# Kernel tuning notes

Hardware: AMD Instinct MI355X
Metric: run time of the kernel (lower is better)

The kernel has to match this reference:

```python
import jax, jax.numpy as jnp
import numpy as np

N_NODES = 50000
N_EDGES = 800000
NODE_FEAT = 3
EDGE_FEAT = 2
EMBED = 64
HIDDEN = 128
LAYERS = 4
POLY = 8


def setup_inputs() -> dict:
    key = jax.random.key(0)
    ks = jax.random.split(key, 24)
    s = 0.05
    inp = {
        "node_features": jax.random.normal(ks[0], (N_NODES, NODE_FEAT), jnp.float32),
        "edge_index": jax.random.randint(ks[1], (2, N_EDGES), 0, N_NODES, jnp.int32),
        "edge_features": jax.random.normal(ks[2], (N_EDGES, EDGE_FEAT), jnp.float32),
        "n": N_NODES,
        # node encoder MLP
        "enc_w1": jax.random.normal(ks[3], (NODE_FEAT, HIDDEN), jnp.float32) * s,
        "enc_b1": jnp.zeros((HIDDEN,), jnp.float32),
        "enc_w2": jax.random.normal(ks[4], (HIDDEN, EMBED), jnp.float32) * s,
        "enc_b2": jnp.zeros((EMBED,), jnp.float32),
        # per-layer conv message MLP (stacked over layers)
        "conv_w1": jax.random.normal(ks[5], (LAYERS, 2 * EMBED + EDGE_FEAT, EMBED), jnp.float32) * s,
        "conv_b1": jnp.zeros((LAYERS, EMBED), jnp.float32),
        "conv_w2": jax.random.normal(ks[6], (LAYERS, EMBED, EMBED), jnp.float32) * s,
        "conv_b2": jnp.zeros((LAYERS, EMBED), jnp.float32),
        # per-layer skip linear and layernorm
        "skip_w": jax.random.normal(ks[7], (LAYERS, EMBED, EMBED), jnp.float32) * s,
        "skip_b": jnp.zeros((LAYERS, EMBED), jnp.float32),
        "ln_g": jnp.ones((LAYERS, EMBED), jnp.float32),
        "ln_b": jnp.zeros((LAYERS, EMBED), jnp.float32),
        # polynomial head
        "head_w1": jax.random.normal(ks[8], (EMBED, EMBED), jnp.float32) * s,
        "head_b1": jnp.zeros((EMBED,), jnp.float32),
        "head_w2": jnp.zeros((EMBED, POLY), jnp.float32),  # zero-init per module
        "head_b2": jnp.ones((POLY,), jnp.float32),         # bias filled with 1.0
    }
    return inp


def _layernorm(x, g, b, eps=1e-5):
    mu = jnp.mean(x, axis=-1, keepdims=True)
    var = jnp.var(x, axis=-1, keepdims=True)
    return (x - mu) * jax.lax.rsqrt(var + eps) * g + b


def reference(node_features, edge_index, edge_features, n,
              enc_w1, enc_b1, enc_w2, enc_b2,
              conv_w1, conv_b1, conv_w2, conv_b2,
              skip_w, skip_b, ln_g, ln_b,
              head_w1, head_b1, head_w2, head_b2):
    rows, cols = edge_index[0], edge_index[1]
    # node encoder
    h = jax.nn.relu(node_features @ enc_w1 + enc_b1) @ enc_w2 + enc_b2  # [n, E]
    L = conv_w1.shape[0]
    for i in range(L):
        # gather + concat: [E_edges, 2*embed + edge_feat]
        msg_in = jnp.concatenate([h[rows], h[cols], edge_features], axis=-1)
        msg = jax.nn.relu(msg_in @ conv_w1[i] + conv_b1[i]) @ conv_w2[i] + conv_b2[i]
        agg = jax.ops.segment_sum(msg, rows, num_segments=n)  # scatter_add over source rows
        h_new = agg + h @ skip_w[i] + skip_b[i]
        h = jax.nn.relu(_layernorm(h_new, ln_g[i], ln_b[i]))
    # polynomial head
    return jax.nn.relu(h @ head_w1 + head_b1) @ head_w2 + head_b2  # [n, poly_degree]
```

## Files before the change

### kernel.cpp

```cpp
#include <hip/hip_runtime.h>

typedef unsigned short u16;
typedef __attribute__((ext_vector_type(8))) short bf16x8;
typedef __attribute__((ext_vector_type(4))) float f32x4;

#define MFMA16(a,b,c) __builtin_amdgcn_mfma_f32_16x16x32_bf16((a),(b),(c),0,0,0)

static __device__ __forceinline__ u16 f2bf(float x){
    unsigned int u = __float_as_uint(x);
    u += 0x7FFFu + ((u >> 16) & 1u);
    return (u16)(u >> 16);
}
static __device__ __forceinline__ float bf2f(short s){
    return __uint_as_float(((unsigned int)(u16)s) << 16);
}

static __device__ __forceinline__ bf16x8 load_bfrag(const float* __restrict__ W, int ldn, int n, int k0){
    bf16x8 r;
    #pragma unroll
    for (int j = 0; j < 8; ++j) r[j] = (short)f2bf(W[(k0 + j) * ldn + n]);
    return r;
}

__global__ __launch_bounds__(256) void enc_kernel(
    const float* __restrict__ X, const float* __restrict__ W1, const float* __restrict__ B1,
    const float* __restrict__ W2, const float* __restrict__ B2,
    const float* __restrict__ cW1, const float* __restrict__ cB1,
    u16* __restrict__ hbf, u16* __restrict__ Ubf, u16* __restrict__ Vbf, int N)
{
    __shared__ u16 sHid[64 * 136];
    __shared__ u16 sH[64 * 72];
    const int tid = threadIdx.x;
    const int w = tid >> 6, l = tid & 63, l15 = l & 15, quad = l >> 4;

    bf16x8 bW[4][4];
    #pragma unroll
    for (int ks = 0; ks < 4; ++ks)
        #pragma unroll
        for (int f = 0; f < 4; ++f)
            bW[ks][f] = load_bfrag(W2, 64, f * 16 + l15, ks * 32 + quad * 8);
    float b2v[4];
    #pragma unroll
    for (int f = 0; f < 4; ++f) b2v[f] = B2[f * 16 + l15];

    const int nbase = blockIdx.x * 64 + w * 16;

    {
        int e = l >> 2;
        int node = nbase + e; if (node > N - 1) node = N - 1;
        float x0 = X[node * 3], x1 = X[node * 3 + 1], x2 = X[node * 3 + 2];
        int k0 = (l & 3) * 32;
        u16* dst = sHid + (w * 16 + e) * 136 + k0;
        #pragma unroll
        for (int j = 0; j < 32; ++j){
            int k = k0 + j;
            float hv = x0 * W1[k] + x1 * W1[128 + k] + x2 * W1[256 + k] + B1[k];
            dst[j] = f2bf(hv > 0.f ? hv : 0.f);
        }
    }

    f32x4 acc[4];
    #pragma unroll
    for (int f = 0; f < 4; ++f){ acc[f][0]=b2v[f]; acc[f][1]=b2v[f]; acc[f][2]=b2v[f]; acc[f][3]=b2v[f]; }
    #pragma unroll
    for (int ks = 0; ks < 4; ++ks){
        bf16x8 a = *(const bf16x8*)&sHid[(w * 16 + l15) * 136 + ks * 32 + quad * 8];
        #pragma unroll
        for (int f = 0; f < 4; ++f) acc[f] = MFMA16(a, bW[ks][f], acc[f]);
    }
    #pragma unroll
    for (int r = 0; r < 4; ++r){
        int node = nbase + quad * 4 + r;
        #pragma unroll
        for (int f = 0; f < 4; ++f){
            u16 hb = f2bf(acc[f][r]);
            sH[(w * 16 + quad * 4 + r) * 72 + f * 16 + l15] = hb;
            if (node < N) hbf[(size_t)node * 64 + f * 16 + l15] = hb;
        }
    }

    bf16x8 bA[2][4], bB[2][4];
    #pragma unroll
    for (int kk = 0; kk < 2; ++kk)
        #pragma unroll
        for (int f = 0; f < 4; ++f){
            int n = f * 16 + l15, k0 = kk * 32 + quad * 8;
            bA[kk][f] = load_bfrag(cW1,           64, n, k0);
            bB[kk][f] = load_bfrag(cW1 + 64 * 64, 64, n, k0);
        }
    float b1n[4];
    #pragma unroll
    for (int f = 0; f < 4; ++f) b1n[f] = cB1[f * 16 + l15];

    bf16x8 a0 = *(const bf16x8*)&sH[(w * 16 + l15) * 72 + quad * 8];
    bf16x8 a1 = *(const bf16x8*)&sH[(w * 16 + l15) * 72 + 32 + quad * 8];

    f32x4 ua[4], va[4];
    #pragma unroll
    for (int f = 0; f < 4; ++f){
        ua[f][0]=b1n[f]; ua[f][1]=b1n[f]; ua[f][2]=b1n[f]; ua[f][3]=b1n[f];
        va[f][0]=0.f; va[f][1]=0.f; va[f][2]=0.f; va[f][3]=0.f;
    }
    #pragma unroll
    for (int f = 0; f < 4; ++f){ ua[f] = MFMA16(a0, bA[0][f], ua[f]); va[f] = MFMA16(a0, bB[0][f], va[f]); }
    #pragma unroll
    for (int f = 0; f < 4; ++f){ ua[f] = MFMA16(a1, bA[1][f], ua[f]); va[f] = MFMA16(a1, bB[1][f], va[f]); }

    #pragma unroll
    for (int r = 0; r < 4; ++r){
        int node = nbase + quad * 4 + r;
        if (node < N){
            #pragma unroll
            for (int f = 0; f < 4; ++f){
                Ubf[(size_t)node * 64 + f * 16 + l15] = f2bf(ua[f][r]);
                Vbf[(size_t)node * 64 + f * 16 + l15] = f2bf(va[f][r]);
            }
        }
    }
}

__global__ __launch_bounds__(256) void countB_kernel(const int* __restrict__ rows,
                                                     int* __restrict__ countsB, int E, int NB){
    __shared__ int c[1024];
    for (int i = threadIdx.x; i < NB; i += 256) c[i] = 0;
    __syncthreads();
    for (int i = blockIdx.x * 256 + threadIdx.x; i < E; i += gridDim.x * 256)
        atomicAdd(&c[rows[i] >> 6], 1);
    __syncthreads();
    for (int i = threadIdx.x; i < NB; i += 256){
        int v = c[i];
        if (v) atomicAdd(&countsB[i], v);
    }
}

__global__ __launch_bounds__(1024) void scanB_kernel(const int* __restrict__ countsB,
                                                     int* __restrict__ offsets,
                                                     int* __restrict__ cursorB, int NB){
    __shared__ int sc[1024];
    const int tid = threadIdx.x;
    int x = (tid < NB) ? countsB[tid] : 0;
    sc[tid] = x;
    __syncthreads();
    for (int d = 1; d < 1024; d <<= 1){
        int v = (tid >= d) ? sc[tid - d] : 0;
        __syncthreads();
        sc[tid] += v;
        __syncthreads();
    }
    int excl = sc[tid] - x;
    if (tid < NB){ offsets[tid] = excl; cursorB[tid] = excl; }
    if (tid == NB - 1) offsets[NB] = sc[tid];
}

#define CHUNK 8192

__global__ __launch_bounds__(1024) void binpack_kernel(
    const int* __restrict__ rows, const int* __restrict__ cols,
    const float* __restrict__ EF, int* __restrict__ cursorB,
    uint2* __restrict__ erec, int E)
{
    __shared__ u16 sRow[CHUNK];
    __shared__ u16 sPerm[CHUNK];
    __shared__ int cntA[1024], cntE[1024], cntC[1024], baseB[1024], sc[1024];
    const int tid = threadIdx.x;
    const int cbase = blockIdx.x * CHUNK;
    int C = E - cbase; if (C > CHUNK) C = CHUNK;
    if (C <= 0) return;

    cntA[tid] = 0;
    __syncthreads();
    for (int k = tid; k < C; k += 1024){
        int r = rows[cbase + k];
        sRow[k] = (u16)r;
        atomicAdd(&cntA[r >> 6], 1);
    }
    __syncthreads();
    sc[tid] = cntA[tid];
    __syncthreads();
    for (int d = 1; d < 1024; d <<= 1){
        int v = (tid >= d) ? sc[tid - d] : 0;
        __syncthreads();
        sc[tid] += v;
        __syncthreads();
    }
    int excl = sc[tid] - cntA[tid];
    cntE[tid] = excl;
    cntC[tid] = excl;
    if (cntA[tid] > 0) baseB[tid] = atomicAdd(&cursorB[tid], cntA[tid]);
    __syncthreads();
    for (int k = tid; k < C; k += 1024){
        int b = sRow[k] >> 6;
        int p = atomicAdd(&cntC[b], 1);
        sPerm[p] = (u16)k;
    }
    __syncthreads();
    for (int p = tid; p < C; p += 1024){
        int k = sPerm[p];
        int i = cbase + k;
        int r = sRow[k];
        int b = r >> 6;
        float2 ef = *(const float2*)&EF[2 * i];
        uint2 v;
        v.x = (unsigned)r | ((unsigned)cols[i] << 16);
        v.y = (unsigned)f2bf(ef.x) | ((unsigned)f2bf(ef.y) << 16);
        erec[baseB[b] + (p - cntE[b])] = v;
    }
}

#define ISSUE_UV(recv, U0, U1, V0, V1) do {                                  \
    int rr_ = (int)((recv).x & 0xFFFFu); if (rr_ == 0xFFFF) rr_ = 0;         \
    int cc_ = (int)((recv).x >> 16);                                         \
    const u16* pu_ = Ubf + (size_t)rr_ * 64 + quad * 8;                      \
    const u16* pv_ = Vbf + (size_t)cc_ * 64 + quad * 8;                      \
    U0 = *(const bf16x8*)(pu_);                                              \
    U1 = *(const bf16x8*)(pu_ + 32);                                         \
    V0 = *(const bf16x8*)(pv_);                                              \
    V1 = *(const bf16x8*)(pv_ + 32);                                         \
} while (0)

static __device__ __forceinline__ unsigned cvtpk(float a, float b){
    unsigned d;
    asm("v_cvt_pk_bf16_f32 %0, %1, %2" : "=v"(d) : "v"(a), "v"(b));
    return d;
}
#define PACK8(dst, x) do {                                                   \
    union { bf16x8 v; unsigned int d[4]; } _u;                               \
    _u.d[0] = cvtpk(x[0], x[1]); _u.d[1] = cvtpk(x[2], x[3]);                \
    _u.d[2] = cvtpk(x[4], x[5]); _u.d[3] = cvtpk(x[6], x[7]);                \
    dst = _u.v;                                                              \
} while (0)

__global__ __launch_bounds__(512, 2) void fused_kernel(
    const u16* __restrict__ Ubf, const u16* __restrict__ Vbf,
    const uint2* __restrict__ erec, const int* __restrict__ offsets,
    const float* __restrict__ W1,
    const float* __restrict__ W2, const float* __restrict__ B2,
    u16* __restrict__ hbf,
    const float* __restrict__ SW, const float* __restrict__ SB,
    const float* __restrict__ LG, const float* __restrict__ LB,
    const float* __restrict__ cW1, const float* __restrict__ cB1,
    u16* __restrict__ Un, u16* __restrict__ Vn,
    int N)
{
    __shared__ u16 sMsg[4][64 * 72];
    __shared__ u16 sRow[4][64];
    float* comb = (float*)&sMsg[0][0];
    u16*   sH   = &sMsg[0][8704];

    const int tid = threadIdx.x;
    const int w = tid >> 6, l = tid & 63, l15 = l & 15, quad = l >> 4;
    const int wq = w & 3, grp = w >> 2;
    const int wq16 = wq * 16;

    bf16x8 bW2[2][4];
    #pragma unroll
    for (int kk = 0; kk < 2; ++kk)
        #pragma unroll
        for (int f = 0; f < 4; ++f)
            bW2[kk][f] = load_bfrag(W2, 64, f * 16 + l15, kk * 32 + quad * 8);
    float bias2[4];
    #pragma unroll
    for (int f = 0; f < 4; ++f) bias2[f] = B2[f * 16 + l15];

    const float* Wc0 = W1 + 128 * 64;
    const float* Wc1 = W1 + 129 * 64;
    bf16x8 e0lo, e0hi, e1lo, e1hi;
    #pragma unroll
    for (int j = 0; j < 8; ++j){
        int kl = quad * 8 + j;
        e0lo[j] = (short)f2bf(Wc0[kl]);      e0hi[j] = (short)f2bf(Wc0[32 + kl]);
        e1lo[j] = (short)f2bf(Wc1[kl]);      e1hi[j] = (short)f2bf(Wc1[32 + kl]);
    }

    const int b = blockIdx.x;
    const int start = offsets[b], end = offsets[b + 1];
    const int nt = (end - start + 63) >> 6;
    const int nr = (nt + 1) >> 1;
    const int tgtrow = wq16 + l15;

    f32x4 aggC[4] = {};

    auto LOADREC = [&](int t) -> uint2 {
        int e = start + t * 64 + wq16 + l15;
        if (e < end) return erec[e];
        uint2 s; s.x = 0x0000FFFFu; s.y = 0u; return s;
    };

    if (nr > 0){
        uint2 recA = LOADREC(grp);
        uint2 recB = LOADREC(grp + 2);
        bf16x8 u0, u1, v0, v1;
        ISSUE_UV(recA, u0, u1, v0, v1);

        for (int r = 0; r < nr; ++r){
            uint2 recC = LOADREC(2 * r + grp + 4);
            bf16x8 nu0, nu1, nv0, nv1;
            ISSUE_UV(recB, nu0, nu1, nv0, nv1);

            int rn_raw = (int)(recA.x & 0xFFFFu);
            float ef0 = bf2f((short)(recA.y & 0xFFFFu));
            float ef1 = bf2f((short)(recA.y >> 16));

            float xl[8], xh[8];
            #pragma unroll
            for (int j = 0; j < 8; ++j){
                float hA = fmaf(ef1, bf2f(e1lo[j]), ef0 * bf2f(e0lo[j]));
                float hB = fmaf(ef1, bf2f(e1hi[j]), ef0 * bf2f(e0hi[j]));
                xl[j] = fmaxf(hA + bf2f(u0[j]) + bf2f(v0[j]), 0.f);
                xh[j] = fmaxf(hB + bf2f(u1[j]) + bf2f(v1[j]), 0.f);
            }
            bf16x8 a0, a1;
            PACK8(a0, xl);
            PACK8(a1, xh);

            f32x4 m[4];
            #pragma unroll
            for (int f = 0; f < 4; ++f){ m[f][0]=bias2[f]; m[f][1]=bias2[f]; m[f][2]=bias2[f]; m[f][3]=bias2[f]; }
            #pragma unroll
            for (int f = 0; f < 4; ++f) m[f] = MFMA16(a0, bW2[0][f], m[f]);
            #pragma unroll
            for (int f = 0; f < 4; ++f) m[f] = MFMA16(a1, bW2[1][f], m[f]);

            const int bi = grp * 2 + (r & 1);
            #pragma unroll
            for (int f = 0; f < 4; ++f){
                uint2 wv;
                wv.x = cvtpk(m[f][0], m[f][1]);
                wv.y = cvtpk(m[f][2], m[f][3]);
                *(uint2*)&sMsg[bi][(f * 16 + l15) * 72 + wq16 + quad * 4] = wv;
            }
            if (quad == 0)
                sRow[bi][wq16 + l15] = (rn_raw == 0xFFFF) ? (u16)0xFFFF : (u16)(rn_raw & 63);

            __syncthreads();

            #pragma unroll
            for (int c = 0; c < 2; ++c){
                union { bf16x8 v; unsigned d[4]; } sfr;
                union { uint4 q; unsigned d[4]; } rv;
                rv.q = *(const uint4*)&sRow[bi][c * 32 + quad * 8];
                #pragma unroll
                for (int k = 0; k < 4; ++k){
                    unsigned d = rv.d[k];
                    unsigned lo = d & 0xFFFFu, hi = d >> 16;
                    sfr.d[k] = (lo == (unsigned)tgtrow ? 0x3F80u : 0u)
                             | (hi == (unsigned)tgtrow ? 0x3F800000u : 0u);
                }
                #pragma unroll
                for (int f = 0; f < 4; ++f){
                    bf16x8 mb = *(const bf16x8*)&sMsg[bi][(f * 16 + l15) * 72 + c * 32 + quad * 8];
                    aggC[f] = MFMA16(sfr.v, mb, aggC[f]);
                }
            }

            recA = recB; recB = recC;
            u0 = nu0; u1 = nu1; v0 = nv0; v1 = nv1;
        }
    }

    __syncthreads();
    if (grp == 1){
        #pragma unroll
        for (int f = 0; f < 4; ++f)
            #pragma unroll
            for (int r = 0; r < 4; ++r)
                comb[(wq16 + quad * 4 + r) * 68 + f * 16 + l15] = aggC[f][r];
    }
    __syncthreads();

    const int nbase = b * 64 + wq16;

    if (grp == 0){
        #pragma unroll
        for (int f = 0; f < 4; ++f)
            #pragma unroll
            for (int r = 0; r < 4; ++r)
                aggC[f][r] += comb[(wq16 + quad * 4 + r) * 68 + f * 16 + l15];

        bf16x8 bW[2][4];
        #pragma unroll
        for (int kk = 0; kk < 2; ++kk)
            #pragma unroll
            for (int f = 0; f < 4; ++f)
                bW[kk][f] = load_bfrag(SW, 64, f * 16 + l15, kk * 32 + quad * 8);
        float sb[4], lg[4], lb[4];
        #pragma unroll
        for (int f = 0; f < 4; ++f){
            int n = f * 16 + l15;
            sb[f] = SB[n]; lg[f] = LG[n]; lb[f] = LB[n];
        }

        int na = nbase + l15; if (na > N - 1) na = N - 1;
        const u16* pa = hbf + (size_t)na * 64 + quad * 8;
        bf16x8 h0 = *(const bf16x8*)pa;
        bf16x8 h1 = *(const bf16x8*)(pa + 32);

        f32x4 acc[4] = {};
        #pragma unroll
        for (int f = 0; f < 4; ++f) acc[f] = MFMA16(h0, bW[0][f], acc[f]);
        #pragma unroll
        for (int f = 0; f < 4; ++f) acc[f] = MFMA16(h1, bW[1][f], acc[f]);

        float vals[4][4];
        #pragma unroll
        for (int r = 0; r < 4; ++r)
            #pragma unroll
            for (int f = 0; f < 4; ++f)
                vals[f][r] = acc[f][r] + sb[f] + aggC[f][r];

        #pragma unroll
        for (int r = 0; r < 4; ++r){
            float s  = vals[0][r] + vals[1][r] + vals[2][r] + vals[3][r];
            float sq = vals[0][r]*vals[0][r] + vals[1][r]*vals[1][r]
                     + vals[2][r]*vals[2][r] + vals[3][r]*vals[3][r];
            #pragma unroll
            for (int msk = 1; msk < 16; msk <<= 1){
                s  += __shfl_xor(s,  msk);
                sq += __shfl_xor(sq, msk);
            }
            float mean = s * (1.f / 64.f);
            float var  = sq * (1.f / 64.f) - mean * mean;
            float rstd = rsqrtf(var + 1e-5f);
            int node = nbase + quad * 4 + r;
            #pragma unroll
            for (int f = 0; f < 4; ++f){
                float hv = (vals[f][r] - mean) * rstd * lg[f] + lb[f];
                hv = hv > 0.f ? hv : 0.f;
                u16 hb = f2bf(hv);
                sH[(wq16 + quad * 4 + r) * 72 + f * 16 + l15] = hb;
                if (node < N) hbf[(size_t)node * 64 + f * 16 + l15] = hb;
            }
        }
    }
    __syncthreads();

    if (cW1){
        const float* Wsel = (grp == 0) ? cW1 : (cW1 + 64 * 64);
        bf16x8 bS[2][4];
        #pragma unroll
        for (int kk = 0; kk < 2; ++kk)
            #pragma unroll
            for (int f = 0; f < 4; ++f)
                bS[kk][f] = load_bfrag(Wsel, 64, f * 16 + l15, kk * 32 + quad * 8);
        float b1n[4];
        #pragma unroll
        for (int f = 0; f < 4; ++f) b1n[f] = (grp == 0) ? cB1[f * 16 + l15] : 0.f;

        bf16x8 a0 = *(const bf16x8*)&sH[(wq16 + l15) * 72 + quad * 8];
        bf16x8 a1 = *(const bf16x8*)&sH[(wq16 + l15) * 72 + 32 + quad * 8];

        f32x4 oa[4];
        #pragma unroll
        for (int f = 0; f < 4; ++f){ oa[f][0]=b1n[f]; oa[f][1]=b1n[f]; oa[f][2]=b1n[f]; oa[f][3]=b1n[f]; }
        #pragma unroll
        for (int f = 0; f < 4; ++f) oa[f] = MFMA16(a0, bS[0][f], oa[f]);
        #pragma unroll
        for (int f = 0; f < 4; ++f) oa[f] = MFMA16(a1, bS[1][f], oa[f]);

        u16* dst = (grp == 0) ? Un : Vn;
        #pragma unroll
        for (int r = 0; r < 4; ++r){
            int node = nbase + quad * 4 + r;
            if (node < N){
                #pragma unroll
                for (int f = 0; f < 4; ++f)
                    dst[(size_t)node * 64 + f * 16 + l15] = f2bf(oa[f][r]);
            }
        }
    }
}

__global__ __launch_bounds__(256) void head_kernel(
    const u16* __restrict__ hbf,
    const float* __restrict__ W1, const float* __restrict__ B1,
    const float* __restrict__ W2, const float* __restrict__ B2,
    float* __restrict__ out, int N)
{
    __shared__ u16 sT[64 * 72];
    const int tid = threadIdx.x;
    const int w = tid >> 6, l = tid & 63, l15 = l & 15, quad = l >> 4;

    bf16x8 bW1[2][4];
    #pragma unroll
    for (int kk = 0; kk < 2; ++kk)
        #pragma unroll
        for (int f = 0; f < 4; ++f)
            bW1[kk][f] = load_bfrag(W1, 64, f * 16 + l15, kk * 32 + quad * 8);
    float b1v[4];
    #pragma unroll
    for (int f = 0; f < 4; ++f) b1v[f] = B1[f * 16 + l15];

    bf16x8 bW2[2];
    #pragma unroll
    for (int kk = 0; kk < 2; ++kk)
        #pragma unroll
        for (int j = 0; j < 8; ++j){
            int k = kk * 32 + quad * 8 + j;
            bW2[kk][j] = (l15 < 8) ? (short)f2bf(W2[k * 8 + l15]) : (short)0;
        }
    float b2v = (l15 < 8) ? B2[l15] : 0.f;

    const int nbase = blockIdx.x * 64 + w * 16;
    int na = nbase + l15; if (na > N - 1) na = N - 1;
    const u16* pa = hbf + (size_t)na * 64 + quad * 8;
    bf16x8 a0 = *(const bf16x8*)pa;
    bf16x8 a1 = *(const bf16x8*)(pa + 32);

    f32x4 acc[4];
    #pragma unroll
    for (int f = 0; f < 4; ++f){ acc[f][0]=b1v[f]; acc[f][1]=b1v[f]; acc[f][2]=b1v[f]; acc[f][3]=b1v[f]; }
    #pragma unroll
    for (int f = 0; f < 4; ++f) acc[f] = MFMA16(a0, bW1[0][f], acc[f]);
    #pragma unroll
    for (int f = 0; f < 4; ++f) acc[f] = MFMA16(a1, bW1[1][f], acc[f]);

    u16* myT = sT + (w * 16) * 72;
    #pragma unroll
    for (int f = 0; f < 4; ++f)
        #pragma unroll
        for (int r = 0; r < 4; ++r){
            float v = acc[f][r] > 0.f ? acc[f][r] : 0.f;
            myT[(quad * 4 + r) * 72 + f * 16 + l15] = f2bf(v);
        }

    f32x4 o = { b2v, b2v, b2v, b2v };
    #pragma unroll
    for (int kk = 0; kk < 2; ++kk){
        bf16x8 a = *(const bf16x8*)&myT[l15 * 72 + kk * 32 + quad * 8];
        o = MFMA16(a, bW2[kk], o);
    }
    #pragma unroll
    for (int r = 0; r < 4; ++r){
        int node = nbase + quad * 4 + r;
        if (node < N && l15 < 8)
            out[(size_t)node * 8 + l15] = o[r];
    }
}

extern "C" void kernel_launch(void* const* d_in, const int* in_sizes, int n_in,
                              void* d_out, int out_size, void* d_ws, size_t ws_size,
                              hipStream_t stream)
{
    const float* X      = (const float*)d_in[0];
    const int*   EI     = (const int*)d_in[1];
    const float* EF     = (const float*)d_in[2];
    const float* encW1  = (const float*)d_in[4];
    const float* encB1  = (const float*)d_in[5];
    const float* encW2  = (const float*)d_in[6];
    const float* encB2  = (const float*)d_in[7];
    const float* convW1 = (const float*)d_in[8];
    const float* convB1 = (const float*)d_in[9];
    const float* convW2 = (const float*)d_in[10];
    const float* convB2 = (const float*)d_in[11];
    const float* skipW  = (const float*)d_in[12];
    const float* skipB  = (const float*)d_in[13];
    const float* lnG    = (const float*)d_in[14];
    const float* lnB    = (const float*)d_in[15];
    const float* headW1 = (const float*)d_in[16];
    const float* headB1 = (const float*)d_in[17];
    const float* headW2 = (const float*)d_in[18];
    const float* headB2 = (const float*)d_in[19];

    const int N = in_sizes[0] / 3;
    const int E = in_sizes[1] / 2;
    const int L = in_sizes[8] / (130 * 64);
    const int* rows = EI;
    const int* cols = EI + E;

    const int NB = (N + 63) / 64;

    auto align256 = [](size_t x){ return (x + 255) & ~(size_t)255; };
    char* p = (char*)d_ws;
    u16* hbf   = (u16*)p;           p += align256((size_t)N * 64 * 2);
    u16* Ubuf0 = (u16*)p;           p += align256((size_t)N * 64 * 2);
    u16* Vbuf0 = (u16*)p;           p += align256((size_t)N * 64 * 2);
    u16* Ubuf1 = (u16*)p;           p += align256((size_t)N * 64 * 2);
    u16* Vbuf1 = (u16*)p;           p += align256((size_t)N * 64 * 2);
    uint2* erec = (uint2*)p;        p += align256((size_t)E * 8);
    int* countsB = (int*)p;         p += align256(1024 * 4);
    int* offsets = (int*)p;         p += align256(1032 * 4);
    int* cursorB = (int*)p;         p += align256(1024 * 4);

    hipMemsetAsync(countsB, 0, (size_t)NB * sizeof(int), stream);
    countB_kernel<<<256, 256, 0, stream>>>(rows, countsB, E, NB);
    scanB_kernel<<<1, 1024, 0, stream>>>(countsB, offsets, cursorB, NB);
    binpack_kernel<<<(E + CHUNK - 1) / CHUNK, 1024, 0, stream>>>(rows, cols, EF, cursorB, erec, E);

    enc_kernel<<<NB, 256, 0, stream>>>(X, encW1, encB1, encW2, encB2,
                                       convW1, convB1, hbf, Ubuf0, Vbuf0, N);

    u16* Ucur = Ubuf0; u16* Vcur = Vbuf0;
    u16* Ualt = Ubuf1; u16* Valt = Vbuf1;
    for (int li = 0; li < L; ++li){
        const float* w1n = (li + 1 < L) ? convW1 + (size_t)(li + 1) * 130 * 64 : nullptr;
        const float* b1n = (li + 1 < L) ? convB1 + (li + 1) * 64 : nullptr;
        fused_kernel<<<NB, 512, 0, stream>>>(Ucur, Vcur, erec, offsets,
            convW1 + (size_t)li * 130 * 64,
            convW2 + (size_t)li * 64 * 64, convB2 + li * 64,
            hbf,
            skipW + (size_t)li * 64 * 64, skipB + li * 64,
            lnG + li * 64, lnB + li * 64,
            w1n, b1n, Ualt, Valt, N);
        u16* t;
        t = Ucur; Ucur = Ualt; Ualt = t;
        t = Vcur; Vcur = Valt; Valt = t;
    }
    head_kernel<<<NB, 256, 0, stream>>>(hbf, headW1, headB1, headW2, headB2,
                                        (float*)d_out, N);
}
```

Measured before the change: 382.0 us.

## Halve node bin size to 32, shrink fused blocks, use persistent grid

Edges are now binned by 32-node groups instead of 64. The fused per-layer kernel processes one 32-node bin per iteration with 256 threads, looping over bins in a persistent grid capped at 1024 blocks. The bin-count scan is rewritten as a wavefront-shuffle scan that handles more than 1024 bins, and binpack handles two bins per thread. The aim is better load balance and occupancy, at the cost of more bins, a second loop level, and the edge-scatter MFMA using only 32 target rows per tile.

```diff
diff --git a/kernel.cpp b/kernel.cpp
--- a/kernel.cpp
+++ b/kernel.cpp
@@ -120,14 +120,14 @@
 }
 
 __global__ __launch_bounds__(256) void countB_kernel(const int* __restrict__ rows,
-                                                     int* __restrict__ countsB, int E, int NB){
-    __shared__ int c[1024];
-    for (int i = threadIdx.x; i < NB; i += 256) c[i] = 0;
+                                                     int* __restrict__ countsB, int E, int NB2){
+    __shared__ int c[2048];
+    for (int i = threadIdx.x; i < 2048; i += 256) c[i] = 0;
     __syncthreads();
     for (int i = blockIdx.x * 256 + threadIdx.x; i < E; i += gridDim.x * 256)
-        atomicAdd(&c[rows[i] >> 6], 1);
-    __syncthreads();
-    for (int i = threadIdx.x; i < NB; i += 256){
+        atomicAdd(&c[rows[i] >> 5], 1);
+    __syncthreads();
+    for (int i = threadIdx.x; i < NB2; i += 256){
         int v = c[i];
         if (v) atomicAdd(&countsB[i], v);
     }
@@ -135,21 +135,41 @@
 
 __global__ __launch_bounds__(1024) void scanB_kernel(const int* __restrict__ countsB,
                                                      int* __restrict__ offsets,
-                                                     int* __restrict__ cursorB, int NB){
-    __shared__ int sc[1024];
-    const int tid = threadIdx.x;
-    int x = (tid < NB) ? countsB[tid] : 0;
-    sc[tid] = x;
-    __syncthreads();
-    for (int d = 1; d < 1024; d <<= 1){
-        int v = (tid >= d) ? sc[tid - d] : 0;
-        __syncthreads();
-        sc[tid] += v;
-        __syncthreads();
-    }
-    int excl = sc[tid] - x;
-    if (tid < NB){ offsets[tid] = excl; cursorB[tid] = excl; }
-    if (tid == NB - 1) offsets[NB] = sc[tid];
+                                                     int* __restrict__ cursorB, int n)
+{
+    __shared__ int wsum[16];
+    __shared__ int carry_s;
+    const int tid = threadIdx.x, lane = tid & 63, wv = tid >> 6;
+    if (tid == 0) carry_s = 0;
+    __syncthreads();
+    for (int base = 0; base < n; base += 1024){
+        int i = base + tid;
+        int x = (i < n) ? countsB[i] : 0;
+        int inc = x;
+        #pragma unroll
+        for (int d = 1; d < 64; d <<= 1){
+            int t = __shfl_up(inc, d);
+            if (lane >= d) inc += t;
+        }
+        if (lane == 63) wsum[wv] = inc;
+        __syncthreads();
+        if (tid < 16){
+            int s = wsum[tid], si = s;
+            #pragma unroll
+            for (int d = 1; d < 16; d <<= 1){
+                int t = __shfl_up(si, d);
+                if (tid >= d) si += t;
+            }
+            wsum[tid] = si - s;
+        }
+        __syncthreads();
+        int excl = inc - x + wsum[wv] + carry_s;
+        if (i < n){ offsets[i] = excl; cursorB[i] = excl; }
+        if (i == n - 1) offsets[n] = excl + x;
+        __syncthreads();
+        if (tid == 1023) carry_s += wsum[15] + inc;
+        __syncthreads();
+    }
 }
 
 #define CHUNK 8192
@@ -161,36 +181,53 @@
 {
     __shared__ u16 sRow[CHUNK];
     __shared__ u16 sPerm[CHUNK];
-    __shared__ int cntA[1024], cntE[1024], cntC[1024], baseB[1024], sc[1024];
-    const int tid = threadIdx.x;
+    __shared__ int cntA[2048];
+    __shared__ int cntC[2048];
+    __shared__ int baseB[2048];
+    __shared__ u16 cntE[2048];
+    __shared__ int wsum[16];
+    const int tid = threadIdx.x, lane = tid & 63, wv = tid >> 6;
     const int cbase = blockIdx.x * CHUNK;
     int C = E - cbase; if (C > CHUNK) C = CHUNK;
     if (C <= 0) return;
 
-    cntA[tid] = 0;
+    cntA[tid] = 0; cntA[tid + 1024] = 0;
     __syncthreads();
     for (int k = tid; k < C; k += 1024){
         int r = rows[cbase + k];
         sRow[k] = (u16)r;
-        atomicAdd(&cntA[r >> 6], 1);
-    }
-    __syncthreads();
-    sc[tid] = cntA[tid];
-    __syncthreads();
-    for (int d = 1; d < 1024; d <<= 1){
-        int v = (tid >= d) ? sc[tid - d] : 0;
-        __syncthreads();
-        sc[tid] += v;
-        __syncthreads();
-    }
-    int excl = sc[tid] - cntA[tid];
-    cntE[tid] = excl;
-    cntC[tid] = excl;
-    if (cntA[tid] > 0) baseB[tid] = atomicAdd(&cursorB[tid], cntA[tid]);
+        atomicAdd(&cntA[r >> 5], 1);
+    }
+    __syncthreads();
+    int a = cntA[2 * tid], bq = cntA[2 * tid + 1];
+    int x = a + bq;
+    int inc = x;
+    #pragma unroll
+    for (int d = 1; d < 64; d <<= 1){
+        int t = __shfl_up(inc, d);
+        if (lane >= d) inc += t;
+    }
+    if (lane == 63) wsum[wv] = inc;
+    __syncthreads();
+    if (tid < 16){
+        int s = wsum[tid], si = s;
+        #pragma unroll
+        for (int d = 1; d < 16; d <<= 1){
+            int t = __shfl_up(si, d);
+            if (tid >= d) si += t;
+        }
+        wsum[tid] = si - s;
+    }
+    __syncthreads();
+    int excl = inc - x + wsum[wv];
+    cntE[2 * tid] = (u16)excl;       cntE[2 * tid + 1] = (u16)(excl + a);
+    cntC[2 * tid] = excl;            cntC[2 * tid + 1] = excl + a;
+    if (a  > 0) baseB[2 * tid]     = atomicAdd(&cursorB[2 * tid],     a);
+    if (bq > 0) baseB[2 * tid + 1] = atomicAdd(&cursorB[2 * tid + 1], bq);
     __syncthreads();
     for (int k = tid; k < C; k += 1024){
-        int b = sRow[k] >> 6;
-        int p = atomicAdd(&cntC[b], 1);
+        int bk = sRow[k] >> 5;
+        int p = atomicAdd(&cntC[bk], 1);
         sPerm[p] = (u16)k;
     }
     __syncthreads();
@@ -198,12 +235,12 @@
         int k = sPerm[p];
         int i = cbase + k;
         int r = sRow[k];
-        int b = r >> 6;
+        int bk = r >> 5;
         float2 ef = *(const float2*)&EF[2 * i];
         uint2 v;
         v.x = (unsigned)r | ((unsigned)cols[i] << 16);
         v.y = (unsigned)f2bf(ef.x) | ((unsigned)f2bf(ef.y) << 16);
-        erec[baseB[b] + (p - cntE[b])] = v;
+        erec[baseB[bk] + (p - (int)cntE[bk])] = v;
     }
 }
 
@@ -230,7 +267,7 @@
     dst = _u.v;                                                              \
 } while (0)
 
-__global__ __launch_bounds__(512, 2) void fused_kernel(
+__global__ __launch_bounds__(256) void fused_kernel(
     const u16* __restrict__ Ubf, const u16* __restrict__ Vbf,
     const uint2* __restrict__ erec, const int* __restrict__ offsets,
     const float* __restrict__ W1,
@@ -240,24 +277,24 @@
     const float* __restrict__ LG, const float* __restrict__ LB,
     const float* __restrict__ cW1, const float* __restrict__ cB1,
     u16* __restrict__ Un, u16* __restrict__ Vn,
-    int N)
+    int N, int NB2)
 {
-    __shared__ u16 sMsg[4][64 * 72];
-    __shared__ u16 sRow[4][64];
+    __shared__ u16 sMsg[4][64 * 40];
+    __shared__ u16 sRowT[4][32];
     float* comb = (float*)&sMsg[0][0];
-    u16*   sH   = &sMsg[0][8704];
+    u16*   sH   = &sMsg[2][0];
 
     const int tid = threadIdx.x;
     const int w = tid >> 6, l = tid & 63, l15 = l & 15, quad = l >> 4;
-    const int wq = w & 3, grp = w >> 2;
-    const int wq16 = wq * 16;
-
-    bf16x8 bW2[2][4];
+    const int pair = w >> 1, pw = w & 1;
+    const int pw16 = pw * 16;
+
+    bf16x8 bW2f[2][4];
     #pragma unroll
     for (int kk = 0; kk < 2; ++kk)
         #pragma unroll
         for (int f = 0; f < 4; ++f)
-            bW2[kk][f] = load_bfrag(W2, 64, f * 16 + l15, kk * 32 + quad * 8);
+            bW2f[kk][f] = load_bfrag(W2, 64, f * 16 + l15, kk * 32 + quad * 8);
     float bias2[4];
     #pragma unroll
     for (int f = 0; f < 4; ++f) bias2[f] = B2[f * 16 + l15];
@@ -272,201 +309,202 @@
         e1lo[j] = (short)f2bf(Wc1[kl]);      e1hi[j] = (short)f2bf(Wc1[32 + kl]);
     }
 
-    const int b = blockIdx.x;
-    const int start = offsets[b], end = offsets[b + 1];
-    const int nt = (end - start + 63) >> 6;
-    const int nr = (nt + 1) >> 1;
-    const int tgtrow = wq16 + l15;
-
-    f32x4 aggC[4] = {};
-
-    auto LOADREC = [&](int t) -> uint2 {
-        int e = start + t * 64 + wq16 + l15;
-        if (e < end) return erec[e];
-        uint2 s; s.x = 0x0000FFFFu; s.y = 0u; return s;
-    };
-
-    if (nr > 0){
-        uint2 recA = LOADREC(grp);
-        uint2 recB = LOADREC(grp + 2);
-        bf16x8 u0, u1, v0, v1;
-        ISSUE_UV(recA, u0, u1, v0, v1);
-
-        for (int r = 0; r < nr; ++r){
-            uint2 recC = LOADREC(2 * r + grp + 4);
-            bf16x8 nu0, nu1, nv0, nv1;
-            ISSUE_UV(recB, nu0, nu1, nv0, nv1);
-
-            int rn_raw = (int)(recA.x & 0xFFFFu);
-            float ef0 = bf2f((short)(recA.y & 0xFFFFu));
-            float ef1 = bf2f((short)(recA.y >> 16));
-
-            float xl[8], xh[8];
-            #pragma unroll
-            for (int j = 0; j < 8; ++j){
-                float hA = fmaf(ef1, bf2f(e1lo[j]), ef0 * bf2f(e0lo[j]));
-                float hB = fmaf(ef1, bf2f(e1hi[j]), ef0 * bf2f(e0hi[j]));
-                xl[j] = fmaxf(hA + bf2f(u0[j]) + bf2f(v0[j]), 0.f);
-                xh[j] = fmaxf(hB + bf2f(u1[j]) + bf2f(v1[j]), 0.f);
+    const int tgtrow = pw16 + l15;
+
+    for (int b = blockIdx.x; b < NB2; b += gridDim.x){
+        const int start = offsets[b], end = offsets[b + 1];
+        const int nt = (end - start + 31) >> 5;
+        const int nr = (nt + 1) >> 1;
+
+        f32x4 aggC[4] = {};
+
+        if (nr > 0){
+            auto LOADREC = [&](int t) -> uint2 {
+                int e = start + t * 32 + pw16 + l15;
+                if (e < end) return erec[e];
+                uint2 s; s.x = 0x0000FFFFu; s.y = 0u; return s;
+            };
+            uint2 recA = LOADREC(pair);
+            uint2 recB = LOADREC(pair + 2);
+            bf16x8 u0, u1, v0, v1;
+            ISSUE_UV(recA, u0, u1, v0, v1);
+
+            for (int r = 0; r < nr; ++r){
+                uint2 recC = LOADREC(2 * r + pair + 4);
+                bf16x8 nu0, nu1, nv0, nv1;
+                ISSUE_UV(recB, nu0, nu1, nv0, nv1);
+
+                int rn_raw = (int)(recA.x & 0xFFFFu);
+                float ef0 = bf2f((short)(recA.y & 0xFFFFu));
+                float ef1 = bf2f((short)(recA.y >> 16));
+
+                float xl[8], xh[8];
+                #pragma unroll
+                for (int j = 0; j < 8; ++j){
+                    float hA = fmaf(ef1, bf2f(e1lo[j]), ef0 * bf2f(e0lo[j]));
+                    float hB = fmaf(ef1, bf2f(e1hi[j]), ef0 * bf2f(e0hi[j]));
+                    xl[j] = fmaxf(hA + bf2f(u0[j]) + bf2f(v0[j]), 0.f);
+                    xh[j] = fmaxf(hB + bf2f(u1[j]) + bf2f(v1[j]), 0.f);
+                }
+                bf16x8 a0, a1;
+                PACK8(a0, xl);
+                PACK8(a1, xh);
+
+                f32x4 m[4];
+                #pragma unroll
+                for (int f = 0; f < 4; ++f){ m[f][0]=bias2[f]; m[f][1]=bias2[f]; m[f][2]=bias2[f]; m[f][3]=bias2[f]; }
+                #pragma unroll
+                for (int f = 0; f < 4; ++f) m[f] = MFMA16(a0, bW2f[0][f], m[f]);
+                #pragma unroll
+                for (int f = 0; f < 4; ++f) m[f] = MFMA16(a1, bW2f[1][f], m[f]);
+
+                const int bi = pair * 2 + (r & 1);
+                #pragma unroll
+                for (int f = 0; f < 4; ++f){
+                    uint2 wv;
+                    wv.x = cvtpk(m[f][0], m[f][1]);
+                    wv.y = cvtpk(m[f][2], m[f][3]);
+                    *(uint2*)&sMsg[bi][(f * 16 + l15) * 40 + pw16 + quad * 4] = wv;
+                }
+                if (quad == 0)
+                    sRowT[bi][pw16 + l15] = (rn_raw == 0xFFFF) ? (u16)0xFFFF : (u16)(rn_raw & 31);
+
+                __syncthreads();
+
+                {
+                    union { bf16x8 v; unsigned d[4]; } sfr;
+                    union { uint4 q; unsigned d[4]; } rv;
+                    rv.q = *(const uint4*)&sRowT[bi][quad * 8];
+                    #pragma unroll
+                    for (int k = 0; k < 4; ++k){
+                        unsigned d = rv.d[k];
+                        unsigned lo = d & 0xFFFFu, hi = d >> 16;
+                        sfr.d[k] = (lo == (unsigned)tgtrow ? 0x3F80u : 0u)
+                                 | (hi == (unsigned)tgtrow ? 0x3F800000u : 0u);
+                    }
+                    #pragma unroll
+                    for (int f = 0; f < 4; ++f){
+                        bf16x8 mb = *(const bf16x8*)&sMsg[bi][(f * 16 + l15) * 40 + quad * 8];
+                        aggC[f] = MFMA16(sfr.v, mb, aggC[f]);
+                    }
+                }
+
+                recA = recB; recB = recC;
+                u0 = nu0; u1 = nu1; v0 = nv0; v1 = nv1;
             }
-            bf16x8 a0, a1;
-            PACK8(a0, xl);
-            PACK8(a1, xh);
-
-            f32x4 m[4];
-            #pragma unroll
-            for (int f = 0; f < 4; ++f){ m[f][0]=bias2[f]; m[f][1]=bias2[f]; m[f][2]=bias2[f]; m[f][3]=bias2[f]; }
-            #pragma unroll
-            for (int f = 0; f < 4; ++f) m[f] = MFMA16(a0, bW2[0][f], m[f]);
-            #pragma unroll
-            for (int f = 0; f < 4; ++f) m[f] = MFMA16(a1, bW2[1][f], m[f]);
-
-            const int bi = grp * 2 + (r & 1);
+        }
+
+        __syncthreads();
+        if (pair == 1){
+            #pragma unroll
+            for (int f = 0; f < 4; ++f)
+                #pragma unroll
+                for (int rr = 0; rr < 4; ++rr)
+                    comb[(pw16 + quad * 4 + rr) * 68 + f * 16 + l15] = aggC[f][rr];
+        }
+        __syncthreads();
+
+        const int nbase = b * 32 + pw16;
+
+        if (pair == 0){
+            #pragma unroll
+            for (int f = 0; f < 4; ++f)
+                #pragma unroll
+                for (int rr = 0; rr < 4; ++rr)
+                    aggC[f][rr] += comb[(pw16 + quad * 4 + rr) * 68 + f * 16 + l15];
+
+            bf16x8 bW[2][4];
+            #pragma unroll
+            for (int kk = 0; kk < 2; ++kk)
+                #pragma unroll
+                for (int f = 0; f < 4; ++f)
+                    bW[kk][f] = load_bfrag(SW, 64, f * 16 + l15, kk * 32 + quad * 8);
+            float sb[4], lg[4], lb[4];
             #pragma unroll
             for (int f = 0; f < 4; ++f){
-                uint2 wv;
-                wv.x = cvtpk(m[f][0], m[f][1]);
-                wv.y = cvtpk(m[f][2], m[f][3]);
-                *(uint2*)&sMsg[bi][(f * 16 + l15) * 72 + wq16 + quad * 4] = wv;
+                int n = f * 16 + l15;
+                sb[f] = SB[n]; lg[f] = LG[n]; lb[f] = LB[n];
             }
-            if (quad == 0)
-                sRow[bi][wq16 + l15] = (rn_raw == 0xFFFF) ? (u16)0xFFFF : (u16)(rn_raw & 63);
-
-            __syncthreads();
-
-            #pragma unroll
-            for (int c = 0; c < 2; ++c){
-                union { bf16x8 v; unsigned d[4]; } sfr;
-                union { uint4 q; unsigned d[4]; } rv;
-                rv.q = *(const uint4*)&sRow[bi][c * 32 + quad * 8];
-                #pragma unroll
-                for (int k = 0; k < 4; ++k){
-                    unsigned d = rv.d[k];
-                    unsigned lo = d & 0xFFFFu, hi = d >> 16;
-                    sfr.d[k] = (lo == (unsigned)tgtrow ? 0x3F80u : 0u)
-                             | (hi == (unsigned)tgtrow ? 0x3F800000u : 0u);
+
+            int na = nbase + l15; if (na > N - 1) na = N - 1;
+            const u16* pa = hbf + (size_t)na * 64 + quad * 8;
+            bf16x8 h0 = *(const bf16x8*)pa;
+            bf16x8 h1 = *(const bf16x8*)(pa + 32);
+
+            f32x4 acc[4] = {};
+            #pragma unroll
+            for (int f = 0; f < 4; ++f) acc[f] = MFMA16(h0, bW[0][f], acc[f]);
+            #pragma unroll
+            for (int f = 0; f < 4; ++f) acc[f] = MFMA16(h1, bW[1][f], acc[f]);
+
+            float vals[4][4];
+            #pragma unroll
+            for (int rr = 0; rr < 4; ++rr)
+                #pragma unroll
+                for (int f = 0; f < 4; ++f)
+                    vals[f][rr] = acc[f][rr] + sb[f] + aggC[f][rr];
+
+            #pragma unroll
+            for (int rr = 0; rr < 4; ++rr){
+                float s  = vals[0][rr] + vals[1][rr] + vals[2][rr] + vals[3][rr];
+                float sq = vals[0][rr]*vals[0][rr] + vals[1][rr]*vals[1][rr]
+                         + vals[2][rr]*vals[2][rr] + vals[3][rr]*vals[3][rr];
+                #pragma unroll
+                for (int msk = 1; msk < 16; msk <<= 1){
+                    s  += __shfl_xor(s,  msk);
+                    sq += __shfl_xor(sq, msk);
                 }
+                float mean = s * (1.f / 64.f);
+                float var  = sq * (1.f / 64.f) - mean * mean;
+                float rstd = rsqrtf(var + 1e-5f);
+                int node = nbase + quad * 4 + rr;
                 #pragma unroll
                 for (int f = 0; f < 4; ++f){
-                    bf16x8 mb = *(const bf16x8*)&sMsg[bi][(f * 16 + l15) * 72 + c * 32 + quad * 8];
-                    aggC[f] = MFMA16(sfr.v, mb, aggC[f]);
+                    float hv = (vals[f][rr] - mean) * rstd * lg[f] + lb[f];
+                    hv = hv > 0.f ? hv : 0.f;
+                    u16 hb = f2bf(hv);
+                    sH[(pw16 + quad * 4 + rr) * 72 + f * 16 + l15] = hb;
+                    if (node < N) hbf[(size_t)node * 64 + f * 16 + l15] = hb;
                 }
             }
-
-            recA = recB; recB = recC;
-            u0 = nu0; u1 = nu1; v0 = nv0; v1 = nv1;
-        }
-    }
-
-    __syncthreads();
-    if (grp == 1){
-        #pragma unroll
-        for (int f = 0; f < 4; ++f)
-            #pragma unroll
-            for (int r = 0; r < 4; ++r)
-                comb[(wq16 + quad * 4 + r) * 68 + f * 16 + l15] = aggC[f][r];
-    }
-    __syncthreads();
-
-    const int nbase = b * 64 + wq16;
-
-    if (grp == 0){
-        #pragma unroll
-        for (int f = 0; f < 4; ++f)
-            #pragma unroll
-            for (int r = 0; r < 4; ++r)
-                aggC[f][r] += comb[(wq16 + quad * 4 + r) * 68 + f * 16 + l15];
-
-        bf16x8 bW[2][4];
-        #pragma unroll
-        for (int kk = 0; kk < 2; ++kk)
-            #pragma unroll
-            for (int f = 0; f < 4; ++f)
-                bW[kk][f] = load_bfrag(SW, 64, f * 16 + l15, kk * 32 + quad * 8);
-        float sb[4], lg[4], lb[4];
-        #pragma unroll
-        for (int f = 0; f < 4; ++f){
-            int n = f * 16 + l15;
-            sb[f] = SB[n]; lg[f] = LG[n]; lb[f] = LB[n];
-        }
-
-        int na = nbase + l15; if (na > N - 1) na = N - 1;
-        const u16* pa = hbf + (size_t)na * 64 + quad * 8;
-        bf16x8 h0 = *(const bf16x8*)pa;
-        bf16x8 h1 = *(const bf16x8*)(pa + 32);
-
-        f32x4 acc[4] = {};
-        #pragma unroll
-        for (int f = 0; f < 4; ++f) acc[f] = MFMA16(h0, bW[0][f], acc[f]);
-        #pragma unroll
-        for (int f = 0; f < 4; ++f) acc[f] = MFMA16(h1, bW[1][f], acc[f]);
-
-        float vals[4][4];
-        #pragma unroll
-        for (int r = 0; r < 4; ++r)
-            #pragma unroll
-            for (int f = 0; f < 4; ++f)
-                vals[f][r] = acc[f][r] + sb[f] + aggC[f][r];
-
-        #pragma unroll
-        for (int r = 0; r < 4; ++r){
-            float s  = vals[0][r] + vals[1][r] + vals[2][r] + vals[3][r];
-            float sq = vals[0][r]*vals[0][r] + vals[1][r]*vals[1][r]
-                     + vals[2][r]*vals[2][r] + vals[3][r]*vals[3][r];
-            #pragma unroll
-            for (int msk = 1; msk < 16; msk <<= 1){
-                s  += __shfl_xor(s,  msk);
-                sq += __shfl_xor(sq, msk);
+        }
+        __syncthreads();
+
+        if (cW1){
+            const float* Wsel = (pair == 0) ? cW1 : (cW1 + 64 * 64);
+            bf16x8 bS[2][4];
+            #pragma unroll
+            for (int kk = 0; kk < 2; ++kk)
+                #pragma unroll
+                for (int f = 0; f < 4; ++f)
+                    bS[kk][f] = load_bfrag(Wsel, 64, f * 16 + l15, kk * 32 + quad * 8);
+            float b1n[4];
+            #pragma unroll
+            for (int f = 0; f < 4; ++f) b1n[f] = (pair == 0) ? cB1[f * 16 + l15] : 0.f;
+
+            bf16x8 a0 = *(const bf16x8*)&sH[(pw16 + l15) * 72 + quad * 8];
+            bf16x8 a1 = *(const bf16x8*)&sH[(pw16 + l15) * 72 + 32 + quad * 8];
+
+            f32x4 oa[4];
+            #pragma unroll
+            for (int f = 0; f < 4; ++f){ oa[f][0]=b1n[f]; oa[f][1]=b1n[f]; oa[f][2]=b1n[f]; oa[f][3]=b1n[f]; }
+            #pragma unroll
+            for (int f = 0; f < 4; ++f) oa[f] = MFMA16(a0, bS[0][f], oa[f]);
+            #pragma unroll
+            for (int f = 0; f < 4; ++f) oa[f] = MFMA16(a1, bS[1][f], oa[f]);
+
+            u16* dst = (pair == 0) ? Un : Vn;
+            #pragma unroll
+            for (int rr = 0; rr < 4; ++rr){
+                int node = nbase + quad * 4 + rr;
+                if (node < N){
+                    #pragma unroll
+                    for (int f = 0; f < 4; ++f)
+                        dst[(size_t)node * 64 + f * 16 + l15] = f2bf(oa[f][rr]);
+                }
             }
-            float mean = s * (1.f / 64.f);
-            float var  = sq * (1.f / 64.f) - mean * mean;
-            float rstd = rsqrtf(var + 1e-5f);
-            int node = nbase + quad * 4 + r;
-            #pragma unroll
-            for (int f = 0; f < 4; ++f){
-                float hv = (vals[f][r] - mean) * rstd * lg[f] + lb[f];
-                hv = hv > 0.f ? hv : 0.f;
-                u16 hb = f2bf(hv);
-                sH[(wq16 + quad * 4 + r) * 72 + f * 16 + l15] = hb;
-                if (node < N) hbf[(size_t)node * 64 + f * 16 + l15] = hb;
-            }
-        }
-    }
-    __syncthreads();
-
-    if (cW1){
-        const float* Wsel = (grp == 0) ? cW1 : (cW1 + 64 * 64);
-        bf16x8 bS[2][4];
-        #pragma unroll
-        for (int kk = 0; kk < 2; ++kk)
-            #pragma unroll
-            for (int f = 0; f < 4; ++f)
-                bS[kk][f] = load_bfrag(Wsel, 64, f * 16 + l15, kk * 32 + quad * 8);
-        float b1n[4];
-        #pragma unroll
-        for (int f = 0; f < 4; ++f) b1n[f] = (grp == 0) ? cB1[f * 16 + l15] : 0.f;
-
-        bf16x8 a0 = *(const bf16x8*)&sH[(wq16 + l15) * 72 + quad * 8];
-        bf16x8 a1 = *(const bf16x8*)&sH[(wq16 + l15) * 72 + 32 + quad * 8];
-
-        f32x4 oa[4];
-        #pragma unroll
-        for (int f = 0; f < 4; ++f){ oa[f][0]=b1n[f]; oa[f][1]=b1n[f]; oa[f][2]=b1n[f]; oa[f][3]=b1n[f]; }
-        #pragma unroll
-        for (int f = 0; f < 4; ++f) oa[f] = MFMA16(a0, bS[0][f], oa[f]);
-        #pragma unroll
-        for (int f = 0; f < 4; ++f) oa[f] = MFMA16(a1, bS[1][f], oa[f]);
-
-        u16* dst = (grp == 0) ? Un : Vn;
-        #pragma unroll
-        for (int r = 0; r < 4; ++r){
-            int node = nbase + quad * 4 + r;
-            if (node < N){
-                #pragma unroll
-                for (int f = 0; f < 4; ++f)
-                    dst[(size_t)node * 64 + f * 16 + l15] = f2bf(oa[f][r]);
-            }
-        }
+        }
+        __syncthreads();
     }
 }
 
@@ -567,7 +605,8 @@
     const int* rows = EI;
     const int* cols = EI + E;
 
-    const int NB = (N + 63) / 64;
+    const int NB64 = (N + 63) / 64;
+    const int NB2  = (N + 31) / 32;
 
     auto align256 = [](size_t x){ return (x + 255) & ~(size_t)255; };
     char* p = (char*)d_ws;
@@ -577,34 +616,35 @@
     u16* Ubuf1 = (u16*)p;           p += align256((size_t)N * 64 * 2);
     u16* Vbuf1 = (u16*)p;           p += align256((size_t)N * 64 * 2);
     uint2* erec = (uint2*)p;        p += align256((size_t)E * 8);
-    int* countsB = (int*)p;         p += align256(1024 * 4);
-    int* offsets = (int*)p;         p += align256(1032 * 4);
-    int* cursorB = (int*)p;         p += align256(1024 * 4);
-
-    hipMemsetAsync(countsB, 0, (size_t)NB * sizeof(int), stream);
-    countB_kernel<<<256, 256, 0, stream>>>(rows, countsB, E, NB);
-    scanB_kernel<<<1, 1024, 0, stream>>>(countsB, offsets, cursorB, NB);
+    int* countsB = (int*)p;         p += align256(2048 * 4);
+    int* offsets = (int*)p;         p += align256(2056 * 4);
+    int* cursorB = (int*)p;         p += align256(2048 * 4);
+
+    hipMemsetAsync(countsB, 0, (size_t)NB2 * sizeof(int), stream);
+    countB_kernel<<<256, 256, 0, stream>>>(rows, countsB, E, NB2);
+    scanB_kernel<<<1, 1024, 0, stream>>>(countsB, offsets, cursorB, NB2);
     binpack_kernel<<<(E + CHUNK - 1) / CHUNK, 1024, 0, stream>>>(rows, cols, EF, cursorB, erec, E);
 
-    enc_kernel<<<NB, 256, 0, stream>>>(X, encW1, encB1, encW2, encB2,
-                                       convW1, convB1, hbf, Ubuf0, Vbuf0, N);
-
+    enc_kernel<<<NB64, 256, 0, stream>>>(X, encW1, encB1, encW2, encB2,
+                                         convW1, convB1, hbf, Ubuf0, Vbuf0, N);
+
+    const int fgrid = NB2 < 1024 ? NB2 : 1024;
     u16* Ucur = Ubuf0; u16* Vcur = Vbuf0;
     u16* Ualt = Ubuf1; u16* Valt = Vbuf1;
     for (int li = 0; li < L; ++li){
         const float* w1n = (li + 1 < L) ? convW1 + (size_t)(li + 1) * 130 * 64 : nullptr;
         const float* b1n = (li + 1 < L) ? convB1 + (li + 1) * 64 : nullptr;
-        fused_kernel<<<NB, 512, 0, stream>>>(Ucur, Vcur, erec, offsets,
+        fused_kernel<<<fgrid, 256, 0, stream>>>(Ucur, Vcur, erec, offsets,
             convW1 + (size_t)li * 130 * 64,
             convW2 + (size_t)li * 64 * 64, convB2 + li * 64,
             hbf,
             skipW + (size_t)li * 64 * 64, skipB + li * 64,
             lnG + li * 64, lnB + li * 64,
-            w1n, b1n, Ualt, Valt, N);
+            w1n, b1n, Ualt, Valt, N, NB2);
         u16* t;
         t = Ucur; Ucur = Ualt; Ualt = t;
         t = Vcur; Vcur = Valt; Valt = t;
     }
-    head_kernel<<<NB, 256, 0, stream>>>(hbf, headW1, headB1, headW2, headB2,
-                                        (float*)d_out, N);
-}
+    head_kernel<<<NB64, 256, 0, stream>>>(hbf, headW1, headB1, headW2, headB2,
+                                          (float*)d_out, N);
+}
```

Result: slower. 440.3 us (+15.3%).
